# Optimization experiments

Measured on AMD Instinct MI355X. Metric: run time of the kernel, lower is better.

Reference implementation:

```python
import jax, jax.numpy as jnp
import numpy as np

D_EMBED = 1024
N_HEADS = 16
D_HEAD = 64
D_MLP = 4096
SEQ = 2048
BATCH = 2
ALPHA = 1.0


def setup_inputs() -> dict:
    key = jax.random.key(0)
    ks = jax.random.split(key, 7)
    s = ALPHA / np.sqrt(D_EMBED)
    return {
        "x": jax.random.normal(ks[0], (BATCH, SEQ, D_EMBED), jnp.float32),
        "W_K": s * jax.random.normal(ks[1], (N_HEADS, D_HEAD, D_EMBED), jnp.float32),
        "W_Q": s * jax.random.normal(ks[2], (N_HEADS, D_HEAD, D_EMBED), jnp.float32),
        "W_V": s * jax.random.normal(ks[3], (N_HEADS, D_HEAD, D_EMBED), jnp.float32),
        "W_O": s * jax.random.normal(ks[4], (D_EMBED, N_HEADS * D_HEAD), jnp.float32),
        "W_in": s * jax.random.normal(ks[5], (D_MLP, D_EMBED), jnp.float32),
        "b_in": jnp.zeros((D_MLP,), jnp.float32),
        "W_out": s * jax.random.normal(ks[6], (D_EMBED, D_MLP), jnp.float32),
        "b_out": jnp.zeros((D_EMBED,), jnp.float32),
    }


def reference(x, W_K, W_Q, W_V, W_O, W_in, b_in, W_out, b_out):
    b, c_len, _ = x.shape
    d_head = W_K.shape[1]
    # q/k/v: [batch, head, ctx, d_head]
    k = jnp.einsum('ahe,bce->bach', W_K, x)
    q = jnp.einsum('ahe,bce->bach', W_Q, x)
    v = jnp.einsum('ahe,bce->bach', W_V, x)
    # scores[b,a,c,C] = k_c . q_C  (faithful to original index convention)
    scores = jnp.einsum('bach,baCh->bacC', k, q)
    mask = jnp.tril(jnp.ones((c_len, c_len), dtype=x.dtype))  # [c, C]
    masked = scores * mask - 1e10 * (1.0 - mask)
    attn = jax.nn.softmax(masked / np.sqrt(d_head), axis=-1)  # softmax over C (query idx)
    # z[b,a,C,h] = sum_c v[b,a,c,h] * attn[b,a,c,C]
    z = jnp.einsum('bach,bacC->baCh', v, attn)
    z_flat = jnp.transpose(z, (0, 2, 1, 3)).reshape(b, c_len, -1)  # [b, c, a*h]
    attn_out = jnp.einsum('ef,bcf->bce', W_O, z_flat)
    x = x + attn_out
    h = jnp.einsum('me,bce->bcm', W_in, x) + b_in
    h = jax.nn.relu(h)
    mlp_out = jnp.einsum('em,bcm->bce', W_out, h) + b_out
    return x + mlp_out
```

## Files before the change

kernel.cpp:

```cpp
#include <hip/hip_runtime.h>
#include <hip/hip_bf16.h>
#include <cstdint>
#include <cstddef>

typedef __bf16 bf16;
typedef bf16 bf16x4 __attribute__((ext_vector_type(4)));
typedef bf16 bf16x8 __attribute__((ext_vector_type(8)));
typedef float floatx4 __attribute__((ext_vector_type(4)));
typedef float floatx16 __attribute__((ext_vector_type(16)));
typedef unsigned int uint;

#define MFMA16(a, b, c) __builtin_amdgcn_mfma_f32_16x16x32_bf16((a), (b), (c), 0, 0, 0)
#define MFMA32(a, b, c) __builtin_amdgcn_mfma_f32_32x32x16_bf16((a), (b), (c), 0, 0, 0)

#define K2 0.18033688011112042f

__device__ __forceinline__ void async16(const void* g, void* l) {
    __builtin_amdgcn_global_load_lds((const __attribute__((address_space(1))) void*)g,
                                     (__attribute__((address_space(3))) void*)l,
                                     16, 0, 0);
}

__device__ __forceinline__ void stage64s(const bf16* g0, int ldg, bf16* lds, int wave, int lane) {
#pragma unroll
    for (int i = 0; i < 2; ++i) {
        int r0 = wave * 16 + i * 8;
        async16(g0 + (size_t)(r0 + (lane >> 3)) * ldg + ((lane & 7) ^ (lane >> 3)) * 8,
                lds + r0 * 64);
    }
}
__device__ __forceinline__ void stage64q(const bf16* g0, int ldg, bf16* lds, int wave, int lane) {
    int r0 = wave * 8;
    async16(g0 + (size_t)(r0 + (lane >> 3)) * ldg + ((lane & 7) ^ (lane >> 3)) * 8,
            lds + r0 * 64);
}
__device__ __forceinline__ bf16x8 rd64(const bf16* t, int row, int chunk) {
    return *(const bf16x8*)&t[row * 64 + ((chunk ^ (row & 7)) * 8)];
}
__device__ __forceinline__ bf16x8 rd32(const bf16* t, int row, int quad) {
    return *(const bf16x8*)&t[row * 32 + ((quad ^ (row & 3)) * 8)];
}

__device__ __forceinline__ uint pk2(float lo, float hi) {
    union { bf16 h[2]; uint u; } c;
    c.h[0] = (bf16)lo;
    c.h[1] = (bf16)hi;
    return c.u;
}

__global__ __launch_bounds__(256) void cvt_all(const float* __restrict__ x,
                                               const float* __restrict__ WQ,
                                               const float* __restrict__ WK,
                                               const float* __restrict__ WV,
                                               const float* __restrict__ WO,
                                               const float* __restrict__ Win,
                                               const float* __restrict__ Wout,
                                               bf16* __restrict__ xb,
                                               bf16* __restrict__ wqkv,
                                               bf16* __restrict__ wo,
                                               bf16* __restrict__ win,
                                               bf16* __restrict__ wout) {
    int blk = blockIdx.x;
    const float* src;
    bf16* dst;
    int off;
    if (blk < 1024)      { src = WQ;   dst = wqkv;           off = blk; }
    else if (blk < 2048) { src = WK;   dst = wqkv + 1048576; off = blk - 1024; }
    else if (blk < 3072) { src = WV;   dst = wqkv + 2097152; off = blk - 2048; }
    else if (blk < 4096) { src = WO;   dst = wo;             off = blk - 3072; }
    else if (blk < 8192) { src = Win;  dst = win;            off = blk - 4096; }
    else if (blk < 12288){ src = Wout; dst = wout;           off = blk - 8192; }
    else                 { src = x;    dst = xb;             off = blk - 12288; }
    int i = off * 1024 + threadIdx.x * 4;
    float4 v = *(const float4*)(src + i);
    bf16x4 o = {(bf16)v.x, (bf16)v.y, (bf16)v.z, (bf16)v.w};
    *(bf16x4*)(dst + i) = o;
}

template <int EPI, int NACC>
__device__ __forceinline__ void epilogue(floatx4 (&acc)[4][NACC], int m0, int n0,
                                         int wm, int wn, int col, int quad,
                                         float* Cf, bf16* Cb, int ldc,
                                         const float* bias, const float* res) {
#pragma unroll
    for (int mi = 0; mi < 4; ++mi)
#pragma unroll
        for (int ni = 0; ni < NACC; ++ni)
#pragma unroll
            for (int r = 0; r < 4; ++r) {
                int row = m0 + wm + mi * 16 + quad * 4 + r;
                int cc = n0 + wn + ni * 16 + col;
                size_t idx = (size_t)row * ldc + cc;
                float v = acc[mi][ni][r];
                if constexpr (EPI == 0) {
                    Cb[idx] = (bf16)v;
                } else if constexpr (EPI == 1) {
                    v += res[idx];
                    Cf[idx] = v;
                    Cb[idx] = (bf16)v;
                } else if constexpr (EPI == 2) {
                    v += bias[cc];
                    v = fmaxf(v, 0.f);
                    Cb[idx] = (bf16)v;
                } else {
                    v += bias[cc] + Cf[idx];
                    Cf[idx] = v;
                }
            }
}

template <int EPI>
__global__ __launch_bounds__(256) void gemm_pipe(const bf16* __restrict__ A, int lda,
                                                 const bf16* __restrict__ B, int ldb, int K,
                                                 float* __restrict__ Cf, bf16* __restrict__ Cb,
                                                 int ldc, const float* __restrict__ bias,
                                                 const float* __restrict__ res) {
    __shared__ __align__(16) bf16 As[3][128 * 32];
    __shared__ __align__(16) bf16 Bs[3][128 * 32];
    const int tid = threadIdx.x, wave = tid >> 6, lane = tid & 63;
    const int m0 = blockIdx.y * 128, n0 = blockIdx.x * 128;
    const int wm = (wave >> 1) * 64, wn = (wave & 1) * 64;
    const int col = lane & 15, quad = lane >> 4;
    const int cs8 = ((lane & 3) ^ ((lane >> 2) & 3)) * 8;

    floatx4 acc[4][4];
#pragma unroll
    for (int mi = 0; mi < 4; ++mi)
#pragma unroll
        for (int ni = 0; ni < 4; ++ni) acc[mi][ni] = (floatx4){0.f, 0.f, 0.f, 0.f};

    auto stage = [&](int buf, int k0) {
#pragma unroll
        for (int i = 0; i < 2; ++i) {
            int r0 = wave * 32 + i * 16;
            async16(A + (size_t)(m0 + r0 + (lane >> 2)) * lda + k0 + cs8,
                    As[buf] + r0 * 32);
            async16(B + (size_t)(n0 + r0 + (lane >> 2)) * ldb + k0 + cs8,
                    Bs[buf] + r0 * 32);
        }
    };

    const int nk = K / 32;
    stage(0, 0);
    stage(1, 32);
    for (int it = 0; it < nk; ++it) {
        if (it + 1 < nk) asm volatile("s_waitcnt vmcnt(4)" ::: "memory");
        else             asm volatile("s_waitcnt vmcnt(0)" ::: "memory");
        __builtin_amdgcn_s_barrier();
        if (it + 2 < nk) stage((it + 2) % 3, (it + 2) * 32);

        const bf16* as = As[it % 3];
        const bf16* bs = Bs[it % 3];
        bf16x8 af[4], bfr[4];
#pragma unroll
        for (int mi = 0; mi < 4; ++mi) af[mi] = rd32(as, wm + mi * 16 + col, quad);
#pragma unroll
        for (int ni = 0; ni < 4; ++ni) bfr[ni] = rd32(bs, wn + ni * 16 + col, quad);
#pragma unroll
        for (int mi = 0; mi < 4; ++mi)
#pragma unroll
            for (int ni = 0; ni < 4; ++ni)
                acc[mi][ni] = MFMA16(af[mi], bfr[ni], acc[mi][ni]);
    }
    epilogue<EPI, 4>(acc, m0, n0, wm, wn, col, quad, Cf, Cb, ldc, bias, res);
}

template <int EPI>
__global__ __launch_bounds__(256) void gemm97s(const bf16* __restrict__ A, int lda,
                                               const bf16* __restrict__ B, int ldb, int K,
                                               float* __restrict__ Cf, bf16* __restrict__ Cb,
                                               int ldc, const float* __restrict__ bias,
                                               const float* __restrict__ res) {
    __shared__ __align__(16) bf16 As[128 * 64];
    __shared__ __align__(16) bf16 Bs[64 * 64];
    const int tid = threadIdx.x, wave = tid >> 6, lane = tid & 63;
    const int m0 = blockIdx.y * 128, n0 = blockIdx.x * 64;
    const int wm = (wave >> 1) * 64, wn = (wave & 1) * 32;
    const int col = lane & 15, quad = lane >> 4;

    floatx4 acc[4][2];
#pragma unroll
    for (int mi = 0; mi < 4; ++mi)
#pragma unroll
        for (int ni = 0; ni < 2; ++ni) acc[mi][ni] = (floatx4){0.f, 0.f, 0.f, 0.f};

    const int rsub = lane >> 3;
    const int csub = ((lane & 7) ^ rsub) * 8;

    for (int k0 = 0; k0 < K; k0 += 64) {
        __syncthreads();
#pragma unroll
        for (int i = 0; i < 4; ++i) {
            int r0 = wave * 32 + i * 8;
            async16(A + (size_t)(m0 + r0 + rsub) * lda + k0 + csub, As + r0 * 64);
        }
#pragma unroll
        for (int i = 0; i < 2; ++i) {
            int r0 = wave * 16 + i * 8;
            async16(B + (size_t)(n0 + r0 + rsub) * ldb + k0 + csub, Bs + r0 * 64);
        }
        __syncthreads();

#pragma unroll
        for (int ks = 0; ks < 2; ++ks) {
            bf16x8 af[4], bfr[2];
#pragma unroll
            for (int mi = 0; mi < 4; ++mi) {
                int row = wm + mi * 16 + col;
                af[mi] = *(const bf16x8*)&As[row * 64 + (((ks * 4 + quad) ^ (row & 7)) * 8)];
            }
#pragma unroll
            for (int ni = 0; ni < 2; ++ni) {
                int row = wn + ni * 16 + col;
                bfr[ni] = *(const bf16x8*)&Bs[row * 64 + (((ks * 4 + quad) ^ (row & 7)) * 8)];
            }
#pragma unroll
            for (int mi = 0; mi < 4; ++mi)
#pragma unroll
                for (int ni = 0; ni < 2; ++ni)
                    acc[mi][ni] = MFMA16(af[mi], bfr[ni], acc[mi][ni]);
        }
    }
    epilogue<EPI, 2>(acc, m0, n0, wm, wn, col, quad, Cf, Cb, ldc, bias, res);
}

__global__ __launch_bounds__(256) void transpose_v(const bf16* __restrict__ qkv,
                                                   const float* __restrict__ linv,
                                                   bf16* __restrict__ vt) {
    __shared__ bf16 t[64][65];
    const int bh = blockIdx.y, ct = blockIdx.x;
    const int b = bh >> 4, a = bh & 15;
    const float* lv = linv + (size_t)bh * 2048 + ct * 64;
    for (int idx = threadIdx.x; idx < 4096; idx += 256) {
        int c = idx >> 6, h = idx & 63;
        float v = (float)qkv[(size_t)(b * 2048 + ct * 64 + c) * 3072 + 2048 + a * 64 + h];
        t[h][c] = (bf16)(v * lv[c]);
    }
    __syncthreads();
    for (int idx = threadIdx.x; idx < 4096; idx += 256) {
        int h = idx >> 6, c = idx & 63;
        vt[(size_t)(bh * 64 + h) * 2048 + ct * 64 + c] = t[h][c];
    }
}

__global__ __launch_bounds__(512, 4) void attn_stats(const bf16* __restrict__ qkv,
                                                     float* __restrict__ linv) {
    __shared__ __align__(16) bf16 Kt[128 * 64];
    __shared__ __align__(16) bf16 Qt[3][64 * 64];
    __shared__ float red[4][32];
    const int xx = blockIdx.x;
    const int t = (xx & 1) ? (15 - (xx >> 1)) : (xx >> 1);
    const int bh = blockIdx.y;
    const int b = bh >> 4, a = bh & 15;
    const int tid = threadIdx.x, wave = tid >> 6, lane = tid & 63;
    const int l31 = lane & 31, lh = lane >> 5;
    const int kq = wave & 3, qh = wave >> 2;
    const bf16* base = qkv + (size_t)b * 2048 * 3072;
    const int c0 = t * 128;
    const int niter = 2 * t + 2;

    stage64s(base + (size_t)c0 * 3072 + 1024 + a * 64, 3072, Kt, wave, lane);
    stage64q(base + a * 64, 3072, Qt[0], wave, lane);
    stage64q(base + (size_t)64 * 3072 + a * 64, 3072, Qt[1], wave, lane);

    float lrun[16];
#pragma unroll
    for (int r = 0; r < 16; ++r) lrun[r] = 0.f;
    bf16x8 kf[4];

    for (int i = 0; i < niter; ++i) {
        if (i + 1 < niter) asm volatile("s_waitcnt vmcnt(1)" ::: "memory");
        else               asm volatile("s_waitcnt vmcnt(0)" ::: "memory");
        __builtin_amdgcn_s_barrier();
        if (i + 2 < niter)
            stage64q(base + (size_t)(i + 2) * 64 * 3072 + a * 64, 3072,
                     Qt[(i + 2) % 3], wave, lane);
        if (i == 0) {
#pragma unroll
            for (int s = 0; s < 4; ++s) kf[s] = rd64(Kt, 32 * kq + l31, 2 * s + lh);
        }
        const bf16* q = Qt[i % 3];
        bf16x8 qf0 = rd64(q, 32 * qh + l31, 0 + lh);
        bf16x8 qf1 = rd64(q, 32 * qh + l31, 2 + lh);
        bf16x8 qf2 = rd64(q, 32 * qh + l31, 4 + lh);
        bf16x8 qf3 = rd64(q, 32 * qh + l31, 6 + lh);
        floatx16 s0 = (floatx16)0.f, s1 = (floatx16)0.f;
        __builtin_amdgcn_s_setprio(1);
        s0 = MFMA32(kf[0], qf0, s0);
        s1 = MFMA32(kf[2], qf2, s1);
        s0 = MFMA32(kf[1], qf1, s0);
        s1 = MFMA32(kf[3], qf3, s1);
        __builtin_amdgcn_s_setprio(0);
#pragma unroll
        for (int r = 0; r < 16; ++r) {
            float e = __builtin_amdgcn_exp2f((s0[r] + s1[r]) * K2);
            if (i >= niter - 2) {
                int Crel = 64 * (i - 2 * t) + 32 * qh + l31;
                int crel = 32 * kq + (r & 3) + 8 * (r >> 2) + 4 * lh;
                if (Crel > crel) e = 0.f;
            }
            lrun[r] += e;
        }
    }
#pragma unroll
    for (int r = 0; r < 16; ++r) {
        float v = lrun[r];
        v += __shfl_xor(v, 1);
        v += __shfl_xor(v, 2);
        v += __shfl_xor(v, 4);
        v += __shfl_xor(v, 8);
        v += __shfl_xor(v, 16);
        lrun[r] = v;
    }
    if (qh == 1 && l31 == 0) {
#pragma unroll
        for (int r = 0; r < 16; ++r)
            red[kq][(r & 3) + 8 * (r >> 2) + 4 * lh] = lrun[r];
    }
    __syncthreads();
    if (qh == 0 && l31 == 0) {
#pragma unroll
        for (int r = 0; r < 16; ++r) {
            int cr = (r & 3) + 8 * (r >> 2) + 4 * lh;
            linv[(size_t)bh * 2048 + c0 + 32 * kq + cr] = 1.0f / (lrun[r] + red[kq][cr]);
        }
    }
}

__global__ __launch_bounds__(512, 4) void attn_av(const bf16* __restrict__ qkv,
                                                  const bf16* __restrict__ vt,
                                                  bf16* __restrict__ zb) {
    __shared__ __align__(16) char smem[65536];
    bf16* Qt = (bf16*)smem;
    bf16* Kt = (bf16*)(smem + 16384);
    bf16* Vt = (bf16*)(smem + 40960);
    const int xx = blockIdx.x;
    const int t = (xx & 1) ? (15 - (xx >> 1)) : (xx >> 1);
    const int bh = blockIdx.y;
    const int b = bh >> 4, a = bh & 15;
    const int tid = threadIdx.x, wave = tid >> 6, lane = tid & 63;
    const int l31 = lane & 31, lh = lane >> 5;
    const int Cq = wave & 3, cq = wave >> 2;
    const bf16* base = qkv + (size_t)b * 2048 * 3072;
    const int C0 = t * 128;
    const int niter = 32 - 2 * t;

    stage64s(base + (size_t)C0 * 3072 + a * 64, 3072, Qt, wave, lane);
    stage64q(base + (size_t)(2 * t) * 64 * 3072 + 1024 + a * 64, 3072, Kt, wave, lane);
    stage64q(vt + (size_t)bh * 64 * 2048 + 2 * t * 64, 2048, Vt, wave, lane);
    stage64q(base + (size_t)(2 * t + 1) * 64 * 3072 + 1024 + a * 64, 3072, Kt + 4096, wave, lane);
    stage64q(vt + (size_t)bh * 64 * 2048 + (2 * t + 1) * 64, 2048, Vt + 4096, wave, lane);

    floatx16 zacc[2];
    zacc[0] = (floatx16)0.f;
    zacc[1] = (floatx16)0.f;
    bf16x8 qf[4];

    for (int i = 0; i < niter; ++i) {
        const int ct = 2 * t + i;
        if (i + 1 < niter) asm volatile("s_waitcnt vmcnt(2)" ::: "memory");
        else               asm volatile("s_waitcnt vmcnt(0)" ::: "memory");
        __builtin_amdgcn_s_barrier();
        if (i + 2 < niter) {
            stage64q(base + (size_t)(ct + 2) * 64 * 3072 + 1024 + a * 64, 3072,
                     Kt + ((i + 2) % 3) * 4096, wave, lane);
            stage64q(vt + (size_t)bh * 64 * 2048 + (ct + 2) * 64, 2048,
                     Vt + ((i + 2) % 3) * 4096, wave, lane);
        }
        if (i == 0) {
#pragma unroll
            for (int s = 0; s < 4; ++s) qf[s] = rd64(Qt, 32 * Cq + l31, 2 * s + lh);
        }
        const bf16* kt = Kt + (i % 3) * 4096;
        const bf16* vts = Vt + (i % 3) * 4096;

        floatx16 s0 = (floatx16)0.f, s1 = (floatx16)0.f;
        __builtin_amdgcn_s_setprio(1);
        s0 = MFMA32(rd64(kt, 32 * cq + l31, 0 + lh), qf[0], s0);
        s1 = MFMA32(rd64(kt, 32 * cq + l31, 4 + lh), qf[2], s1);
        s0 = MFMA32(rd64(kt, 32 * cq + l31, 2 + lh), qf[1], s0);
        s1 = MFMA32(rd64(kt, 32 * cq + l31, 6 + lh), qf[3], s1);
        __builtin_amdgcn_s_setprio(0);

        float p[16];
#pragma unroll
        for (int r = 0; r < 16; ++r) {
            float e = __builtin_amdgcn_exp2f((s0[r] + s1[r]) * K2);
            if (i < 2) {
                int Crel = 32 * Cq + l31;
                int crel = 64 * i + 32 * cq + (r & 3) + 8 * (r >> 2) + 4 * lh;
                if (Crel > crel) e = 0.f;
            }
            p[r] = e;
        }

        bf16x8 pa[2];
#pragma unroll
        for (int g = 0; g < 2; ++g) {
            uint w0 = pk2(p[8 * g + 0], p[8 * g + 1]);
            uint w1 = pk2(p[8 * g + 2], p[8 * g + 3]);
            uint w2 = pk2(p[8 * g + 4], p[8 * g + 5]);
            uint w3 = pk2(p[8 * g + 6], p[8 * g + 7]);
            uint xw0 = (uint)__shfl_xor((int)w0, 32);
            uint xw1 = (uint)__shfl_xor((int)w1, 32);
            uint xw2 = (uint)__shfl_xor((int)w2, 32);
            uint xw3 = (uint)__shfl_xor((int)w3, 32);
            union { uint u[4]; bf16x8 v; } cv;
            cv.u[0] = lh ? xw2 : w0;
            cv.u[1] = lh ? xw3 : w1;
            cv.u[2] = lh ? w2 : xw0;
            cv.u[3] = lh ? w3 : xw1;
            pa[g] = cv.v;
        }

        __builtin_amdgcn_s_setprio(1);
#pragma unroll
        for (int ht = 0; ht < 2; ++ht) {
#pragma unroll
            for (int s = 0; s < 2; ++s) {
                bf16x8 vf = rd64(vts, 32 * ht + l31, 4 * cq + 2 * s + lh);
                zacc[ht] = MFMA32(pa[s], vf, zacc[ht]);
            }
        }
        __builtin_amdgcn_s_setprio(0);
    }

    __syncthreads();
    float* Zex = (float*)smem;
    if (cq == 1) {
#pragma unroll
        for (int ht = 0; ht < 2; ++ht)
#pragma unroll
            for (int q = 0; q < 4; ++q) {
                float4 t4 = {zacc[ht][4 * q + 0], zacc[ht][4 * q + 1],
                             zacc[ht][4 * q + 2], zacc[ht][4 * q + 3]};
                *(float4*)&Zex[Cq * 2048 + lane * 32 + (((ht * 4 + q) ^ (lane & 7)) * 4)] = t4;
            }
    }
    __syncthreads();
    if (cq == 0) {
#pragma unroll
        for (int ht = 0; ht < 2; ++ht)
#pragma unroll
            for (int q = 0; q < 4; ++q) {
                float4 t4 = *(const float4*)&Zex[Cq * 2048 + lane * 32 +
                                                 (((ht * 4 + q) ^ (lane & 7)) * 4)];
                zacc[ht][4 * q + 0] += t4.x;
                zacc[ht][4 * q + 1] += t4.y;
                zacc[ht][4 * q + 2] += t4.z;
                zacc[ht][4 * q + 3] += t4.w;
            }
#pragma unroll
        for (int ht = 0; ht < 2; ++ht)
#pragma unroll
            for (int r = 0; r < 16; ++r) {
                int Cg = C0 + 32 * Cq + (r & 3) + 8 * (r >> 2) + 4 * lh;
                zb[(size_t)(b * 2048 + Cg) * 1024 + a * 64 + 32 * ht + l31] =
                    (bf16)zacc[ht][r];
            }
    }
}

extern "C" void kernel_launch(void* const* d_in, const int* in_sizes, int n_in,
                              void* d_out, int out_size, void* d_ws, size_t ws_size,
                              hipStream_t stream) {
    (void)in_sizes; (void)n_in; (void)out_size; (void)ws_size;
    const float* x    = (const float*)d_in[0];
    const float* WK   = (const float*)d_in[1];
    const float* WQ   = (const float*)d_in[2];
    const float* WV   = (const float*)d_in[3];
    const float* WO   = (const float*)d_in[4];
    const float* Win  = (const float*)d_in[5];
    const float* bin  = (const float*)d_in[6];
    const float* Wout = (const float*)d_in[7];
    const float* bout = (const float*)d_in[8];
    float* out = (float*)d_out;

    char* ws = (char*)d_ws;
    bf16*  xb   = (bf16*)(ws + 0);
    bf16*  wqkv = (bf16*)(ws + 8388608);
    bf16*  wo   = (bf16*)(ws + 14680064);
    bf16*  win  = (bf16*)(ws + 16777216);
    bf16*  wout = (bf16*)(ws + 25165824);
    bf16*  qkvb = (bf16*)(ws + 33554432);
    bf16*  vtb  = (bf16*)(ws + 58720256);
    float* mst  = (float*)(ws + 67108864);
    bf16*  zbuf = (bf16*)(ws + 67633152);
    bf16*  xmid = (bf16*)(ws + 76021760);
    bf16*  hbuf = (bf16*)(ws + 84410368);

    cvt_all<<<16384, 256, 0, stream>>>(x, WQ, WK, WV, WO, Win, Wout,
                                       xb, wqkv, wo, win, wout);

    gemm_pipe<0><<<dim3(24, 32), 256, 0, stream>>>(xb, 1024, wqkv, 1024, 1024,
                                                   nullptr, qkvb, 3072, nullptr, nullptr);
    attn_stats<<<dim3(16, 32), 512, 0, stream>>>(qkvb, mst);
    transpose_v<<<dim3(32, 32), 256, 0, stream>>>(qkvb, mst, vtb);
    attn_av<<<dim3(16, 32), 512, 0, stream>>>(qkvb, vtb, zbuf);
    gemm97s<1><<<dim3(16, 32), 256, 0, stream>>>(zbuf, 1024, wo, 1024, 1024,
                                                 out, xmid, 1024, nullptr, x);
    gemm_pipe<2><<<dim3(32, 32), 256, 0, stream>>>(xmid, 1024, win, 1024, 1024,
                                                   nullptr, hbuf, 4096, bin, nullptr);
    gemm97s<3><<<dim3(16, 32), 256, 0, stream>>>(hbuf, 4096, wout, 4096, 4096,
                                                 out, nullptr, 1024, bout, nullptr);
}
```

Measured before the change: 381.4 us.

## Triple-buffer async LDS staging and swizzle block order in 128x64 GEMMs

```diff
diff --git a/kernel.cpp b/kernel.cpp
--- a/kernel.cpp
+++ b/kernel.cpp
@@ -166,53 +166,64 @@
 }
 
 template <int EPI>
-__global__ __launch_bounds__(256) void gemm97s(const bf16* __restrict__ A, int lda,
-                                               const bf16* __restrict__ B, int ldb, int K,
-                                               float* __restrict__ Cf, bf16* __restrict__ Cb,
-                                               int ldc, const float* __restrict__ bias,
-                                               const float* __restrict__ res) {
-    __shared__ __align__(16) bf16 As[128 * 64];
-    __shared__ __align__(16) bf16 Bs[64 * 64];
+__global__ __launch_bounds__(256) void gemm_pipe64(const bf16* __restrict__ A, int lda,
+                                                   const bf16* __restrict__ B, int ldb, int K,
+                                                   float* __restrict__ Cf, bf16* __restrict__ Cb,
+                                                   int ldc, const float* __restrict__ bias,
+                                                   const float* __restrict__ res) {
+    __shared__ __align__(16) bf16 As[3][128 * 64];
+    __shared__ __align__(16) bf16 Bs[3][64 * 64];
     const int tid = threadIdx.x, wave = tid >> 6, lane = tid & 63;
-    const int m0 = blockIdx.y * 128, n0 = blockIdx.x * 64;
+    const int orig = blockIdx.y * 16 + blockIdx.x;
+    const int wgid = (orig & 7) * 64 + (orig >> 3);
+    const int m0 = (wgid >> 4) * 128, n0 = (wgid & 15) * 64;
     const int wm = (wave >> 1) * 64, wn = (wave & 1) * 32;
     const int col = lane & 15, quad = lane >> 4;
-
-    floatx4 acc[4][2];
-#pragma unroll
-    for (int mi = 0; mi < 4; ++mi)
-#pragma unroll
-        for (int ni = 0; ni < 2; ++ni) acc[mi][ni] = (floatx4){0.f, 0.f, 0.f, 0.f};
-
     const int rsub = lane >> 3;
     const int csub = ((lane & 7) ^ rsub) * 8;
 
-    for (int k0 = 0; k0 < K; k0 += 64) {
-        __syncthreads();
+    floatx4 acc[4][2];
+#pragma unroll
+    for (int mi = 0; mi < 4; ++mi)
+#pragma unroll
+        for (int ni = 0; ni < 2; ++ni) acc[mi][ni] = (floatx4){0.f, 0.f, 0.f, 0.f};
+
+    auto stage = [&](int buf, int k0) {
 #pragma unroll
         for (int i = 0; i < 4; ++i) {
             int r0 = wave * 32 + i * 8;
-            async16(A + (size_t)(m0 + r0 + rsub) * lda + k0 + csub, As + r0 * 64);
+            async16(A + (size_t)(m0 + r0 + rsub) * lda + k0 + csub, As[buf] + r0 * 64);
         }
 #pragma unroll
         for (int i = 0; i < 2; ++i) {
             int r0 = wave * 16 + i * 8;
-            async16(B + (size_t)(n0 + r0 + rsub) * ldb + k0 + csub, Bs + r0 * 64);
-        }
-        __syncthreads();
-
+            async16(B + (size_t)(n0 + r0 + rsub) * ldb + k0 + csub, Bs[buf] + r0 * 64);
+        }
+    };
+
+    const int nk = K / 64;
+    stage(0, 0);
+    stage(1, 64);
+    for (int it = 0; it < nk; ++it) {
+        if (it + 1 < nk) asm volatile("s_waitcnt vmcnt(6)" ::: "memory");
+        else             asm volatile("s_waitcnt vmcnt(0)" ::: "memory");
+        __builtin_amdgcn_s_barrier();
+        if (it + 2 < nk) stage((it + 2) % 3, (it + 2) * 64);
+
+        const bf16* as = As[it % 3];
+        const bf16* bs = Bs[it % 3];
 #pragma unroll
         for (int ks = 0; ks < 2; ++ks) {
             bf16x8 af[4], bfr[2];
 #pragma unroll
             for (int mi = 0; mi < 4; ++mi) {
                 int row = wm + mi * 16 + col;
-                af[mi] = *(const bf16x8*)&As[row * 64 + (((ks * 4 + quad) ^ (row & 7)) * 8)];
+                af[mi] = *(const bf16x8*)&as[row * 64 + (((ks * 4 + quad) ^ (row & 7)) * 8)];
             }
 #pragma unroll
             for (int ni = 0; ni < 2; ++ni) {
                 int row = wn + ni * 16 + col;
-                bfr[ni] = *(const bf16x8*)&Bs[row * 64 + (((ks * 4 + quad) ^ (row & 7)) * 8)];
+                bfr[ni] = *(const bf16x8*)&bs[row * 64 + (((ks * 4 + quad) ^ (row & 7)) * 8)];
             }
 #pragma unroll
             for (int mi = 0; mi < 4; ++mi)
@@ -497,10 +508,10 @@
     attn_stats<<<dim3(16, 32), 512, 0, stream>>>(qkvb, mst);
     transpose_v<<<dim3(32, 32), 256, 0, stream>>>(qkvb, mst, vtb);
     attn_av<<<dim3(16, 32), 512, 0, stream>>>(qkvb, vtb, zbuf);
-    gemm97s<1><<<dim3(16, 32), 256, 0, stream>>>(zbuf, 1024, wo, 1024, 1024,
-                                                 out, xmid, 1024, nullptr, x);
+    gemm_pipe64<1><<<dim3(16, 32), 256, 0, stream>>>(zbuf, 1024, wo, 1024, 1024,
+                                                     out, xmid, 1024, nullptr, x);
     gemm_pipe<2><<<dim3(32, 32), 256, 0, stream>>>(xmid, 1024, win, 1024, 1024,
                                                    nullptr, hbuf, 4096, bin, nullptr);
-    gemm97s<3><<<dim3(16, 32), 256, 0, stream>>>(hbuf, 4096, wout, 4096, 4096,
-                                                 out, nullptr, 1024, bout, nullptr);
-}
+    gemm_pipe64<3><<<dim3(16, 32), 256, 0, stream>>>(hbuf, 4096, wout, 4096, 4096,
+                                                     out, nullptr, 1024, bout, nullptr);
+}
```

New measurement: 380.2 us. About the same (-0.3%).
